# Kernel optimization log

Hardware: AMD Instinct MI355X
Metric: run time of the kernel (lower is better)

## Reference

```python
import jax, jax.numpy as jnp
import numpy as np

IOU_THR = 0.5    # cfg.MODEL.BOX_TEACHER.IOU_THR
SCORE_THR = 0.05 # cfg.MODEL.BOX_TEACHER.SCORE_THR
M, N, H, W = 100, 20, 800, 800


def _pairwise_iou(b1, b2):
    # b1: [M,4] xyxy, b2: [N,4] xyxy -> [M,N]
    area1 = (b1[:, 2] - b1[:, 0]) * (b1[:, 3] - b1[:, 1])
    area2 = (b2[:, 2] - b2[:, 0]) * (b2[:, 3] - b2[:, 1])
    lt = jnp.maximum(b1[:, None, :2], b2[None, :, :2])
    rb = jnp.minimum(b1[:, None, 2:], b2[None, :, 2:])
    wh = jnp.clip(rb - lt, 0.0)
    inter = wh[..., 0] * wh[..., 1]
    union = area1[:, None] + area2[None, :] - inter
    return inter / jnp.clip(union, 1e-6)


def _greedy_match(iou, scores):
    # Faithful replica of the sequential greedy loop in pseudo_labeling1,
    # including the original `gtm[j] > 0` (not > -1) availability check.
    m_, n_ = iou.shape
    order = jnp.argsort(-scores)  # descending by score
    gt_ids = jnp.arange(n_)

    def step(carry, i):
        gtm, biou = carry
        row = iou[i]
        valid = (gtm <= 0) & (row >= IOU_THR)
        masked = jnp.where(valid, row, -jnp.inf)
        m = jnp.argmax(masked)  # first max, matching `iou_ < max_iou` tie rule
        found = valid.any() & (scores[i] >= SCORE_THR)
        hit = found & (gt_ids == m)
        gtm = jnp.where(hit, i.astype(gtm.dtype), gtm)
        biou = jnp.where(hit, row[m], biou)
        return (gtm, biou), None

    gtm0 = jnp.full((n_,), -1, dtype=jnp.int32)
    (gtm, biou), _ = jax.lax.scan(step, (gtm0, jnp.zeros((n_,), iou.dtype)), order)
    return gtm, biou


def setup_inputs() -> dict:
    key = jax.random.key(0)
    k1, k2, k3, k4, k5, k6 = jax.random.split(key, 6)
    cxcy = jax.random.uniform(k1, (M, 2), minval=150.0, maxval=650.0)
    wh = jax.random.uniform(k2, (M, 2), minval=60.0, maxval=300.0)
    pred_boxes = jnp.concatenate([cxcy - wh / 2, cxcy + wh / 2], axis=1)
    # GT boxes are perturbed copies of the first N preds so matching fires
    gt_boxes = pred_boxes[:N] + jax.random.normal(k3, (N, 4)) * 8.0
    pred_scores = jax.random.uniform(k4, (M,))
    mask_score = jax.random.uniform(k5, (M,))
    pred_masks = jax.random.uniform(k6, (M, H, W))
    return {
        "pred_boxes": pred_boxes,
        "pred_scores": pred_scores,
        "mask_score": mask_score,
        "pred_masks": pred_masks,
        "gt_boxes": gt_boxes,
    }


def reference(pred_boxes, pred_scores, mask_score, pred_masks, gt_boxes):
    iou = _pairwise_iou(pred_boxes, gt_boxes)          # [M,N]
    gtm, biou = _greedy_match(iou, pred_scores)        # [N], [N]
    matched = gtm > -1
    idx = jnp.where(matched, gtm, 0)
    # gt_masks[gtm>-1] = pred_masks[gtm[gtm>-1]]
    gt_bitmasks = jnp.where(matched[:, None, None], pred_masks[idx], 0.0)  # [N,H,W]
    gt_masks_flags = jnp.where(matched, mask_score[idx], 0.0)              # [N]
    out_pred_scores = jnp.where(matched, pred_scores[idx], 0.0)            # [N]
    return gt_bitmasks, gt_masks_flags, out_pred_scores
```

## Files before the change

### kernel.cpp

```cpp
#include <hip/hip_runtime.h>
#include <stdint.h>

#define M_PRED 100
#define N_GT 20
#define IMG_H 800
#define IMG_W 800
#define IOU_THR_F 0.5f
#define SCORE_THR_F 0.05f

__global__ __launch_bounds__(256) void match_kernel(
    const float* __restrict__ pred_boxes,
    const float* __restrict__ pred_scores,
    const float* __restrict__ mask_score,
    const float* __restrict__ gt_boxes,
    float* __restrict__ out_flags,
    float* __restrict__ out_scores,
    int* __restrict__ gtm_out)
{
    __shared__ float s_iou[M_PRED * N_GT];
    __shared__ float s_pb[M_PRED * 4];
    __shared__ float s_gb[N_GT * 4];
    __shared__ float s_scores[M_PRED];
    __shared__ int   s_order[M_PRED];
    __shared__ int   s_cand[M_PRED];
    __shared__ int   s_order2[M_PRED];
    __shared__ int   s_ncand;

    const int tid = threadIdx.x;

    for (int t = tid; t < M_PRED * 4; t += 256) s_pb[t] = pred_boxes[t];
    for (int t = tid; t < N_GT * 4;   t += 256) s_gb[t] = gt_boxes[t];
    for (int t = tid; t < M_PRED;     t += 256) s_scores[t] = pred_scores[t];
    __syncthreads();

    for (int t = tid; t < M_PRED * N_GT; t += 256) {
        int i = t / N_GT, j = t - i * N_GT;
        float ax0 = s_pb[i * 4 + 0], ay0 = s_pb[i * 4 + 1];
        float ax1 = s_pb[i * 4 + 2], ay1 = s_pb[i * 4 + 3];
        float bx0 = s_gb[j * 4 + 0], by0 = s_gb[j * 4 + 1];
        float bx1 = s_gb[j * 4 + 2], by1 = s_gb[j * 4 + 3];
        float area1 = (ax1 - ax0) * (ay1 - ay0);
        float area2 = (bx1 - bx0) * (by1 - by0);
        float lx = fmaxf(ax0, bx0), ly = fmaxf(ay0, by0);
        float rx = fminf(ax1, bx1), ry = fminf(ay1, by1);
        float w = fmaxf(rx - lx, 0.0f), h = fmaxf(ry - ly, 0.0f);
        float inter = w * h;
        float uni = area1 + area2 - inter;
        s_iou[t] = inter / fmaxf(uni, 1e-6f);
    }
    __syncthreads();

    if (tid < M_PRED) {
        float si = s_scores[tid];
        int r = 0;
        for (int k = 0; k < M_PRED; ++k) {
            float sk = s_scores[k];
            r += (sk > si || (sk == si && k < tid)) ? 1 : 0;
        }
        s_order[r] = tid;
        float mx = 0.0f;
        for (int j = 0; j < N_GT; ++j) mx = fmaxf(mx, s_iou[tid * N_GT + j]);
        s_cand[tid] = (si >= SCORE_THR_F && mx >= IOU_THR_F) ? 1 : 0;
    }
    __syncthreads();

    if (tid == 0) {
        int cnt = 0;
        for (int r = 0; r < M_PRED; ++r) {
            int i = s_order[r];
            if (s_cand[i]) s_order2[cnt++] = i;
        }
        s_ncand = cnt;
    }
    __syncthreads();

    if (tid < 64) {
        const int lane = tid;
        const bool is_gt = lane < N_GT;
        int gtm_j = -1;
        const int nc = s_ncand;
        for (int r = 0; r < nc; ++r) {
            int icur = s_order2[r];
            float vr = is_gt ? s_iou[icur * N_GT + lane] : 0.0f;
            bool valid = is_gt && (gtm_j <= 0) && (vr >= IOU_THR_F);
            unsigned long long key = valid
                ? ((((unsigned long long)__float_as_uint(vr)) << 32) |
                   (unsigned long long)(63 - lane))
                : 0ull;
            #pragma unroll
            for (int d = 1; d < 64; d <<= 1) {
                unsigned long long o = __shfl_xor(key, d, 64);
                key = (o > key) ? o : key;
            }
            if (key != 0ull) {
                int bj = 63 - (int)(key & 0xffffffffull);
                if (lane == bj) gtm_j = icur;
            }
        }
        if (is_gt) {
            gtm_out[lane] = gtm_j;
            bool matched = gtm_j > -1;
            int idx = matched ? gtm_j : 0;
            out_flags[lane]  = matched ? mask_score[idx] : 0.0f;
            out_scores[lane] = matched ? s_scores[idx]   : 0.0f;
        }
    }
}

__global__ __launch_bounds__(256) void scatter_kernel(
    const float4* __restrict__ pred_masks,
    const int* __restrict__ gtm,
    float4* __restrict__ out)
{
    const int j = blockIdx.y;
    const int idx = blockIdx.x * 256 + threadIdx.x;
    const int per = (IMG_H * IMG_W) / 4;
    int g = gtm[j];
    float4 v = make_float4(0.0f, 0.0f, 0.0f, 0.0f);
    if (g > -1) v = pred_masks[(size_t)g * per + idx];
    out[(size_t)j * per + idx] = v;
}

extern "C" void kernel_launch(void* const* d_in, const int* in_sizes, int n_in,
                              void* d_out, int out_size, void* d_ws, size_t ws_size,
                              hipStream_t stream) {
    const float* pred_boxes  = (const float*)d_in[0];
    const float* pred_scores = (const float*)d_in[1];
    const float* mask_score  = (const float*)d_in[2];
    const float* pred_masks  = (const float*)d_in[3];
    const float* gt_boxes    = (const float*)d_in[4];
    float* out = (float*)d_out;
    int* gtm_ws = (int*)d_ws;

    float* out_flags  = out + (size_t)N_GT * IMG_H * IMG_W;
    float* out_scores = out_flags + N_GT;

    match_kernel<<<1, 256, 0, stream>>>(pred_boxes, pred_scores, mask_score,
                                        gt_boxes, out_flags, out_scores, gtm_ws);

    dim3 grid((IMG_H * IMG_W / 4) / 256, N_GT);
    scatter_kernel<<<grid, dim3(256), 0, stream>>>(
        (const float4*)pred_masks, gtm_ws, (float4*)out);
}
```

Measured before the change: 334.4 us.

## Use nontemporal loads/stores in scatter and shrink greedy-match reduction

The mask scatter kernel now uses nontemporal load and store builtins on a native float vector type, so the large streaming copy bypasses cache retention. The match kernel shrinks to 128 threads. Its greedy step now does a 32-wide float max shuffle plus a ballot to pick the first max lane, replacing a 64-bit packed key reduction. The match kernel is tiny, so most of any effect would come from the nontemporal streaming path on the bandwidth-bound copy.

```diff
diff --git a/kernel.cpp b/kernel.cpp
--- a/kernel.cpp
+++ b/kernel.cpp
@@ -8,7 +8,9 @@
 #define IOU_THR_F 0.5f
 #define SCORE_THR_F 0.05f
 
-__global__ __launch_bounds__(256) void match_kernel(
+typedef float f32x4 __attribute__((ext_vector_type(4)));
+
+__global__ __launch_bounds__(128) void match_kernel(
     const float* __restrict__ pred_boxes,
     const float* __restrict__ pred_scores,
     const float* __restrict__ mask_score,
@@ -28,12 +30,12 @@
 
     const int tid = threadIdx.x;
 
-    for (int t = tid; t < M_PRED * 4; t += 256) s_pb[t] = pred_boxes[t];
-    for (int t = tid; t < N_GT * 4;   t += 256) s_gb[t] = gt_boxes[t];
-    for (int t = tid; t < M_PRED;     t += 256) s_scores[t] = pred_scores[t];
+    for (int t = tid; t < M_PRED * 4; t += 128) s_pb[t] = pred_boxes[t];
+    if (tid < N_GT * 4) s_gb[tid] = gt_boxes[tid];
+    if (tid < M_PRED)   s_scores[tid] = pred_scores[tid];
     __syncthreads();
 
-    for (int t = tid; t < M_PRED * N_GT; t += 256) {
+    for (int t = tid; t < M_PRED * N_GT; t += 128) {
         int i = t / N_GT, j = t - i * N_GT;
         float ax0 = s_pb[i * 4 + 0], ay0 = s_pb[i * 4 + 1];
         float ax1 = s_pb[i * 4 + 2], ay1 = s_pb[i * 4 + 3];
@@ -74,26 +76,22 @@
     }
     __syncthreads();
 
-    if (tid < 64) {
+    if (tid < 32) {
         const int lane = tid;
         const bool is_gt = lane < N_GT;
         int gtm_j = -1;
         const int nc = s_ncand;
         for (int r = 0; r < nc; ++r) {
             int icur = s_order2[r];
-            float vr = is_gt ? s_iou[icur * N_GT + lane] : 0.0f;
-            bool valid = is_gt && (gtm_j <= 0) && (vr >= IOU_THR_F);
-            unsigned long long key = valid
-                ? ((((unsigned long long)__float_as_uint(vr)) << 32) |
-                   (unsigned long long)(63 - lane))
-                : 0ull;
+            float v = is_gt ? s_iou[icur * N_GT + lane] : -1.0f;
+            bool valid = is_gt && (gtm_j <= 0) && (v >= IOU_THR_F);
+            float x = valid ? v : -1.0f;
             #pragma unroll
-            for (int d = 1; d < 64; d <<= 1) {
-                unsigned long long o = __shfl_xor(key, d, 64);
-                key = (o > key) ? o : key;
-            }
-            if (key != 0ull) {
-                int bj = 63 - (int)(key & 0xffffffffull);
+            for (int d = 1; d < 32; d <<= 1)
+                x = fmaxf(x, __shfl_xor(x, d, 32));
+            unsigned long long mb = __ballot(valid && (v == x));
+            if (mb != 0ull) {
+                int bj = (int)__builtin_ctzll(mb);
                 if (lane == bj) gtm_j = icur;
             }
         }
@@ -108,17 +106,17 @@
 }
 
 __global__ __launch_bounds__(256) void scatter_kernel(
-    const float4* __restrict__ pred_masks,
+    const f32x4* __restrict__ pred_masks,
     const int* __restrict__ gtm,
-    float4* __restrict__ out)
+    f32x4* __restrict__ out)
 {
     const int j = blockIdx.y;
     const int idx = blockIdx.x * 256 + threadIdx.x;
     const int per = (IMG_H * IMG_W) / 4;
     int g = gtm[j];
-    float4 v = make_float4(0.0f, 0.0f, 0.0f, 0.0f);
-    if (g > -1) v = pred_masks[(size_t)g * per + idx];
-    out[(size_t)j * per + idx] = v;
+    f32x4 v = {0.0f, 0.0f, 0.0f, 0.0f};
+    if (g > -1) v = __builtin_nontemporal_load(&pred_masks[(size_t)g * per + idx]);
+    __builtin_nontemporal_store(v, &out[(size_t)j * per + idx]);
 }
 
 extern "C" void kernel_launch(void* const* d_in, const int* in_sizes, int n_in,
@@ -135,10 +133,10 @@
     float* out_flags  = out + (size_t)N_GT * IMG_H * IMG_W;
     float* out_scores = out_flags + N_GT;
 
-    match_kernel<<<1, 256, 0, stream>>>(pred_boxes, pred_scores, mask_score,
+    match_kernel<<<1, 128, 0, stream>>>(pred_boxes, pred_scores, mask_score,
                                         gt_boxes, out_flags, out_scores, gtm_ws);
 
     dim3 grid((IMG_H * IMG_W / 4) / 256, N_GT);
     scatter_kernel<<<grid, dim3(256), 0, stream>>>(
-        (const float4*)pred_masks, gtm_ws, (float4*)out);
+        (const f32x4*)pred_masks, gtm_ws, (f32x4*)out);
 }
```

New measurement: 332.5 us. Within noise of the previous version (-0.6%).
